# Kernel tuning notes

Measured on AMD Instinct MI355X. Metric: run time of the kernel, lower is better.

Reference implementation:

```python
import jax, jax.numpy as jnp
import numpy as np

A_BITS = 4          # a_bits
W_BITS = 4          # w_bits / w_slices (w_slices = 1)
NUM_CHUNKS = 9      # ceil(in_ch*9 / 64) = ceil(576/64)
BN_EPS = 1e-5


def quantize_weight(w, bits):
    # WeightQuantize STE: uniform symmetric quantization, straight-through on clipped range
    n = 2.0 ** (bits - 1) - 1.0
    c = jnp.clip(w, -1.0, 1.0)
    q = jnp.round(c * n) / n
    return c + jax.lax.stop_gradient(q - c)


def create_input_stream(a, a_bits):
    # residual multi-bit binarization into a_bits sign planes, x ~= sum_i plane_i / 2^(i+1)
    x = jnp.clip(a, -1.0, 1.0)
    planes = []
    r = x
    for i in range(a_bits):
        s = jnp.where(r >= 0, 1.0, -1.0)
        planes.append(x + jax.lax.stop_gradient(s - x))  # STE plane
        r = r - s / (2.0 ** (i + 1))
    return jnp.stack(planes, 0)  # [a_bits, B, C*9, L]


def unfold3x3(x, pad=1):
    # torch F.unfold(kernel=3, stride=1) ordering: (C, kh, kw) flattened channel-major
    B, C, H, W = x.shape
    xp = jnp.pad(x, ((0, 0), (0, 0), (pad, pad), (pad, pad)))
    cols = jnp.stack([xp[:, :, i:i + H, j:j + W] for i in range(3) for j in range(3)], axis=2)
    return cols.reshape(B, C * 9, H * W)  # [B, C*9, L]


def mtj(x, gamma, beta, key):
    mean = x.mean(axis=(0, 2), keepdims=True)
    var = x.var(axis=(0, 2), keepdims=True)  # biased, as torch BN
    normed = (x - mean) / jnp.sqrt(var + BN_EPS) * gamma[None, :, None] + beta[None, :, None]
    t = jnp.tanh(4.0 * normed)
    rand = jax.random.uniform(key, x.shape, minval=-1.0, maxval=1.0)
    out = jnp.where(t > rand, 1.0, -1.0)
    out = jnp.where(normed == 0.0, 0.0, out)
    c = jnp.clip(normed, -1.0, 1.0)
    return c + jax.lax.stop_gradient(out - c)


def setup_inputs() -> dict:
    key = jax.random.key(0)
    k1, k2 = jax.random.split(key)
    inputs = jax.random.normal(k1, (8, 64, 32, 32), dtype=jnp.float32)
    weight = jax.random.normal(k2, (128, 64, 3, 3), dtype=jnp.float32) * (2.0 / (64 * 9)) ** 0.5
    gamma = jnp.ones((128,), jnp.float32)
    beta = jnp.zeros((128,), jnp.float32)
    return {"inputs": inputs, "weight": weight, "gamma": gamma, "beta": beta}


def reference(inputs, weight, gamma, beta):
    O = weight.shape[0]
    # weight standardization (per output filter; std is unbiased as torch .std())
    wf = weight.reshape(O, -1)
    bw = weight - wf.mean(-1)[:, None, None, None]
    std = bw.reshape(O, -1).std(-1, ddof=1)
    bw = bw / std[:, None, None, None]
    qw = quantize_weight(bw, W_BITS)                      # [O, C, 3, 3]
    a = unfold3x3(inputs)                                 # [B, C*9, L]
    stream = create_input_stream(a, A_BITS)               # [A, B, C*9, L]
    A, B, CK, L = stream.shape
    cs = CK // NUM_CHUNKS
    x = stream.reshape(A * B, NUM_CHUNKS, cs, L)          # chunked along the C*9 axis
    fw = qw.reshape(O, NUM_CHUNKS, cs)                    # flattened weight chunks
    # per-chunk F.linear, vectorized over chunks: [nc, A*B, O, L]
    lt = jnp.einsum('ngkl,ogk->gnol', x, fw)
    keys = jax.random.split(jax.random.key(42), NUM_CHUNKS)
    pre = jax.vmap(lambda t, k: mtj(t, gamma, beta, k))(lt, keys) / NUM_CHUNKS
    out = pre.sum(0)                                      # sum chunks (w_slices=1 -> identity combine)
    # gen_image_vector_and_sum: recombine activation bit-planes
    out = out.reshape(A, B, O, L)
    wts = (2.0 ** -(jnp.arange(A, dtype=jnp.float32) + 1.0)).reshape(A, 1, 1, 1)
    out = (out * wts).sum(0)
    HW = int(np.sqrt(L))
    return out.reshape(B, O, HW, HW)                      # F.fold with (1,1) kernel
```

## Files before the change

### kernel.cpp

```cpp
#include <hip/hip_runtime.h>
#include <stdint.h>

#ifndef PRNG_PARTITIONABLE
#define PRNG_PARTITIONABLE 1
#endif

#define ONE_M_U 0.99999994039535522461f

__device__ __forceinline__ void tf_4a(uint32_t& x0, uint32_t& x1){
  x0 += x1; x1 = (x1<<13)|(x1>>19); x1 ^= x0;
  x0 += x1; x1 = (x1<<15)|(x1>>17); x1 ^= x0;
  x0 += x1; x1 = (x1<<26)|(x1>>6);  x1 ^= x0;
  x0 += x1; x1 = (x1<<6) |(x1>>26); x1 ^= x0;
}
__device__ __forceinline__ void tf_4b(uint32_t& x0, uint32_t& x1){
  x0 += x1; x1 = (x1<<17)|(x1>>15); x1 ^= x0;
  x0 += x1; x1 = (x1<<29)|(x1>>3);  x1 ^= x0;
  x0 += x1; x1 = (x1<<16)|(x1>>16); x1 ^= x0;
  x0 += x1; x1 = (x1<<24)|(x1>>8);  x1 ^= x0;
}
__device__ __forceinline__ void threefry2x32(uint32_t k0, uint32_t k1, uint32_t& x0, uint32_t& x1){
  uint32_t k2 = k0 ^ k1 ^ 0x1BD11BDAu;
  x0 += k0; x1 += k1;
  tf_4a(x0,x1); x0 += k1; x1 += k2 + 1u;
  tf_4b(x0,x1); x0 += k2; x1 += k0 + 2u;
  tf_4a(x0,x1); x0 += k0; x1 += k1 + 3u;
  tf_4b(x0,x1); x0 += k1; x1 += k2 + 4u;
  tf_4a(x0,x1); x0 += k2; x1 += k0 + 5u;
}

__device__ __forceinline__ float bits_to_unit(uint32_t b){
  #pragma clang fp contract(off)
  float f = __uint_as_float((b >> 9) | 0x3f800000u) - 1.0f;
  float r = f * 2.0f + (-1.0f);
  return __builtin_fmaxf(-1.0f, r);
}

__device__ __forceinline__ float xla_tanh_f32(float x){
  #pragma clang fp contract(off)
  float ax = __builtin_fabsf(x);
  float xc = __builtin_fminf(__builtin_fmaxf(x, -9.0f), 9.0f);
  float x2 = xc * xc;
  float nm = -2.76076847742355e-16f;
  nm = x2 * nm + 2.00018790482477e-13f;
  nm = x2 * nm + -8.60467152213735e-11f;
  nm = x2 * nm + 5.12229709037114e-08f;
  nm = x2 * nm + 1.48572235717979e-05f;
  nm = x2 * nm + 6.37261928875436e-04f;
  nm = x2 * nm + 4.89352455891786e-03f;
  nm = xc * nm;
  float dn = 1.19825839466702e-06f;
  dn = x2 * dn + 1.18534705686654e-04f;
  dn = x2 * dn + 2.26843463243900e-03f;
  dn = x2 * dn + 4.89352518554385e-03f;
  float res = nm / dn;
  return (ax < 0.0004f) ? x : res;
}

__device__ __forceinline__ float dot64(unsigned long long sw, unsigned long long dw,
                                       const float* w){
  float acc = 0.0f;
  #pragma unroll
  for (int k = 0; k < 64; ++k){
    float mag = ((dw >> k) & 1ull) ? ONE_M_U : 1.0f;
    float p   = ((sw >> k) & 1ull) ? mag : -mag;
    acc = __builtin_fmaf(p, w[k], acc);
  }
  return acc;
}

#define QW_OFF   0u
#define SGN_OFF  294912u
#define DIM_OFF  2654208u
#define KEYS_OFF 5013504u
#define MV_OFF   5013632u
#define LT_OFF   5023744u
#define LT_BYTES 150994944u
#define PART_OFF (LT_OFF + LT_BYTES)
#define PART_BYTES 2359296u
#define WS_NEEDED_FAST (PART_OFF + PART_BYTES)

__global__ __launch_bounds__(256) void k_front(const float* __restrict__ X,
        const float* __restrict__ W, float* __restrict__ qw, uint32_t* __restrict__ keys,
        unsigned long long* __restrict__ sgn, unsigned long long* __restrict__ dimw){
  #pragma clang fp contract(off)
  __shared__ float  bwL[576];
  __shared__ double red[64];
  int bx = blockIdx.x;
  int t = threadIdx.x;
  if (bx < 288){
    int g = bx >> 5;
    int tid = (bx & 31) * 256 + t;
    int b = tid >> 10, l = tid & 1023;
    int h = l >> 5, w = l & 31;
    unsigned long long sw0=0ull, sw1=0ull, sw2=0ull, sw3=0ull;
    unsigned long long dw0=0ull, dw1=0ull, dw2=0ull, dw3=0ull;
    const float* Xb = X + b*64*1024;
    int ck0 = g*64;
    #pragma unroll
    for (int i = 0; i < 64; ++i){
      int ck = ck0 + i;
      int c = ck / 9, kp = ck % 9;
      int di = kp / 3 - 1, dj = kp % 3 - 1;
      int hh = h + di, ww = w + dj;
      float v = 0.0f;
      if (hh >= 0 && hh < 32 && ww >= 0 && ww < 32)
        v = Xb[(c*32 + hh)*32 + ww];
      float x = __builtin_fminf(__builtin_fmaxf(v, -1.0f), 1.0f);
      float r = x;
      {
        float sv = (r >= 0.0f) ? 1.0f : -1.0f;
        float d  = sv - x; float p = x + d;
        if (sv > 0.0f) sw0 |= (1ull << i);
        if (__builtin_fabsf(p) < 1.0f) dw0 |= (1ull << i);
        r = r - sv * 0.5f;
      }
      {
        float sv = (r >= 0.0f) ? 1.0f : -1.0f;
        float d  = sv - x; float p = x + d;
        if (sv > 0.0f) sw1 |= (1ull << i);
        if (__builtin_fabsf(p) < 1.0f) dw1 |= (1ull << i);
        r = r - sv * 0.25f;
      }
      {
        float sv = (r >= 0.0f) ? 1.0f : -1.0f;
        float d  = sv - x; float p = x + d;
        if (sv > 0.0f) sw2 |= (1ull << i);
        if (__builtin_fabsf(p) < 1.0f) dw2 |= (1ull << i);
        r = r - sv * 0.125f;
      }
      {
        float sv = (r >= 0.0f) ? 1.0f : -1.0f;
        float d  = sv - x; float p = x + d;
        if (sv > 0.0f) sw3 |= (1ull << i);
        if (__builtin_fabsf(p) < 1.0f) dw3 |= (1ull << i);
        r = r - sv * 0.0625f;
      }
    }
    sgn [((0*8+b)*9 + g)*1024 + l] = sw0;
    sgn [((1*8+b)*9 + g)*1024 + l] = sw1;
    sgn [((2*8+b)*9 + g)*1024 + l] = sw2;
    sgn [((3*8+b)*9 + g)*1024 + l] = sw3;
    dimw[((0*8+b)*9 + g)*1024 + l] = dw0;
    dimw[((1*8+b)*9 + g)*1024 + l] = dw1;
    dimw[((2*8+b)*9 + g)*1024 + l] = dw2;
    dimw[((3*8+b)*9 + g)*1024 + l] = dw3;
  } else {
    int o = bx - 288;
    if (t < 64){
      double s = 0.0;
      for (int j = t; j < 576; j += 64) s += (double)W[o*576 + j];
      red[t] = s;
    }
    __syncthreads();
    for (int k = 32; k > 0; k >>= 1){ if (t < k) red[t] += red[t+k]; __syncthreads(); }
    float mean1 = (float)(red[0] / 576.0);
    __syncthreads();
    for (int j = t; j < 576; j += 256) bwL[j] = W[o*576 + j] - mean1;
    __syncthreads();
    if (t < 64){
      double s = 0.0;
      for (int j = t; j < 576; j += 64) s += (double)bwL[j];
      red[t] = s;
    }
    __syncthreads();
    for (int k = 32; k > 0; k >>= 1){ if (t < k) red[t] += red[t+k]; __syncthreads(); }
    float mean2 = (float)(red[0] / 576.0);
    __syncthreads();
    if (t < 64){
      double s = 0.0;
      for (int j = t; j < 576; j += 64){ float c = bwL[j] - mean2; float sq = c * c; s += (double)sq; }
      red[t] = s;
    }
    __syncthreads();
    for (int k = 32; k > 0; k >>= 1){ if (t < k) red[t] += red[t+k]; __syncthreads(); }
    float varf = (float)(red[0] / 575.0);
    float stdv = __builtin_sqrtf(varf);
    __syncthreads();
    for (int j = t; j < 576; j += 256){
      float b2 = bwL[j] / stdv;
      float c  = __builtin_fminf(__builtin_fmaxf(b2, -1.0f), 1.0f);
      float q  = __builtin_rintf(c * 7.0f) / 7.0f;
      float fwd = c + (q - c);
      int g = j >> 6, k = j & 63;
      qw [(g*128 + o)*64 + k] = fwd;
    }
    if (o == 0 && t == 0){
#if PRNG_PARTITIONABLE
      for (int g = 0; g < 9; ++g){
        uint32_t x0 = 0u, x1 = (uint32_t)g;
        threefry2x32(0u, 42u, x0, x1);
        keys[2*g] = x0; keys[2*g+1] = x1;
      }
#else
      uint32_t outv[18];
      for (int i = 0; i < 9; ++i){
        uint32_t x0 = (uint32_t)i, x1 = (uint32_t)(9 + i);
        threefry2x32(0u, 42u, x0, x1);
        outv[i] = x0; outv[9+i] = x1;
      }
      for (int j = 0; j < 18; ++j) keys[j] = outv[j];
#endif
    }
  }
}

__global__ __launch_bounds__(256) void k_gemm(const float* __restrict__ qw,
        const unsigned long long* __restrict__ sgn, const unsigned long long* __restrict__ dimw,
        float* __restrict__ lt, double* __restrict__ part){
  __shared__ float4 wS[128*17];
  __shared__ float4 pS[128*17];
  int lq = blockIdx.x, g = blockIdx.y, n = blockIdx.z;
  int t = threadIdx.x;
  {
    int o = t >> 4, kq = t & 15;
    const float4* qw4 = (const float4*)qw;
    #pragma unroll
    for (int i = 0; i < 8; ++i){
      int oo = o + 16*i;
      wS[oo*17 + kq] = qw4[(g*128 + oo)*16 + kq];
    }
  }
  {
    int l = t >> 1, kh = t & 1;
    unsigned long long sw = sgn [(n*9+g)*1024 + lq*128 + l];
    unsigned long long dw = dimw[(n*9+g)*1024 + lq*128 + l];
    #pragma unroll
    for (int kq = 0; kq < 8; ++kq){
      int kqq = kh*8 + kq;
      float4 v;
      {
        int k = kqq*4;
        float m0 = ((dw>>k)&1ull)?ONE_M_U:1.0f; v.x = ((sw>>k)&1ull)?m0:-m0;
        float m1 = ((dw>>(k+1))&1ull)?ONE_M_U:1.0f; v.y = ((sw>>(k+1))&1ull)?m1:-m1;
        float m2 = ((dw>>(k+2))&1ull)?ONE_M_U:1.0f; v.z = ((sw>>(k+2))&1ull)?m2:-m2;
        float m3 = ((dw>>(k+3))&1ull)?ONE_M_U:1.0f; v.w = ((sw>>(k+3))&1ull)?m3:-m3;
      }
      pS[l*17 + kqq] = v;
    }
  }
  __syncthreads();
  int ot = t >> 4, ltl = t & 15;
  float acc[8][8];
  #pragma unroll
  for (int i = 0; i < 8; ++i)
    #pragma unroll
    for (int j = 0; j < 8; ++j) acc[i][j] = 0.0f;
  for (int kq = 0; kq < 16; ++kq){
    float wr[8][4], pr[8][4];
    #pragma unroll
    for (int i = 0; i < 8; ++i) *(float4*)wr[i] = wS[(ot*8+i)*17 + kq];
    #pragma unroll
    for (int j = 0; j < 8; ++j) *(float4*)pr[j] = pS[(ltl+16*j)*17 + kq];
    #pragma unroll
    for (int e = 0; e < 4; ++e)
      #pragma unroll
      for (int i = 0; i < 8; ++i)
        #pragma unroll
        for (int j = 0; j < 8; ++j)
          acc[i][j] = __builtin_fmaf(pr[j][e], wr[i][e], acc[i][j]);
  }
  #pragma unroll
  for (int i = 0; i < 8; ++i){
    int o = ot*8 + i;
    float* dst = lt + ((size_t)((n*9+g)*128 + o))*1024 + lq*128 + ltl;
    #pragma unroll
    for (int j = 0; j < 8; ++j) dst[16*j] = acc[i][j];
  }
  double ps[8];
  #pragma unroll
  for (int i = 0; i < 8; ++i){
    double s = 0.0;
    #pragma unroll
    for (int j = 0; j < 8; ++j) s += (double)acc[i][j];
    ps[i] = s;
  }
  __syncthreads();
  double* red = (double*)pS;
  #pragma unroll
  for (int i = 0; i < 8; ++i) red[(ot*8+i)*16 + ltl] = ps[i];
  __syncthreads();
  if (t < 128){
    double s = 0.0;
    #pragma unroll
    for (int q = 0; q < 16; ++q) s += red[t*16 + q];
    part[((size_t)g*128 + t)*256 + n*8 + lq] = s;
  }
}

__global__ __launch_bounds__(256) void k_stats(const float* __restrict__ lt,
        const double* __restrict__ part, float* __restrict__ mv){
  #pragma clang fp contract(off)
  __shared__ double redm[64];
  __shared__ double red[256];
  __shared__ float meanS;
  int go = blockIdx.x;
  int g = go >> 7, o = go & 127;
  int t = threadIdx.x;
  if (t < 64){
    double s = 0.0;
    for (int idx = t; idx < 256; idx += 64) s += part[(size_t)go*256 + idx];
    redm[t] = s;
  }
  __syncthreads();
  for (int k = 32; k > 0; k >>= 1){ if (t < k) redm[t] += redm[t+k]; __syncthreads(); }
  if (t == 0){
    float mean = (float)(redm[0] / 32768.0);
    mv[go*2] = mean;
    meanS = mean;
  }
  __syncthreads();
  float mean = meanS;
  double s2 = 0.0;
  #pragma unroll 8
  for (int n = 0; n < 32; ++n){
    const float4* p4 = (const float4*)(lt + ((size_t)((n*9+g)*128 + o)) * 1024);
    float4 v = p4[t];
    { float c = v.x - mean; float sq = c * c; s2 += (double)sq; }
    { float c = v.y - mean; float sq = c * c; s2 += (double)sq; }
    { float c = v.z - mean; float sq = c * c; s2 += (double)sq; }
    { float c = v.w - mean; float sq = c * c; s2 += (double)sq; }
  }
  red[t] = s2; __syncthreads();
  for (int k = 128; k > 0; k >>= 1){ if (t < k) red[t] += red[t+k]; __syncthreads(); }
  if (t == 0){
    float var = (float)(red[0] / 32768.0);
    mv[go*2 + 1] = __builtin_sqrtf(var + 1e-5f);
  }
}

__global__ __launch_bounds__(256) void k_out_fast(const float* __restrict__ lt,
        const float* __restrict__ mv, const uint32_t* __restrict__ keys,
        const float* __restrict__ gamma, const float* __restrict__ beta,
        float* __restrict__ out){
  #pragma clang fp contract(off)
  __shared__ float    mvL[18];
  __shared__ uint32_t kL[18];
  int bi = blockIdx.x;
  int lc = bi & 3, o = (bi >> 2) & 127, b = bi >> 9;
  int t = threadIdx.x;
  if (t < 18){ mvL[t] = mv[((t>>1)*128 + o)*2 + (t&1)]; kL[t] = keys[t]; }
  __syncthreads();
  int l = lc*256 + t;
  float gma = gamma[o], bta = beta[o];
  float S[4] = {0.0f, 0.0f, 0.0f, 0.0f};
  for (int g = 0; g < 9; ++g){
    float rnd[4];
#if PRNG_PARTITIONABLE
    #pragma unroll
    for (int a = 0; a < 4; ++a){
      uint32_t m = (uint32_t)((a*8 + b)*131072 + o*1024 + l);
      uint32_t x0 = 0u, x1 = m;
      threefry2x32(kL[2*g], kL[2*g+1], x0, x1);
      rnd[a] = bits_to_unit(x0 ^ x1);
    }
#else
    #pragma unroll
    for (int a01 = 0; a01 < 2; ++a01){
      uint32_t m = (uint32_t)((a01*8 + b)*131072 + o*1024 + l);
      uint32_t x0 = m, x1 = m + 2097152u;
      threefry2x32(kL[2*g], kL[2*g+1], x0, x1);
      rnd[a01]     = bits_to_unit(x0);
      rnd[a01 + 2] = bits_to_unit(x1);
    }
#endif
    float mean = mvL[2*g], den = mvL[2*g+1];
    #pragma unroll
    for (int a = 0; a < 4; ++a){
      int n = a*8 + b;
      float tv = lt[((size_t)((n*9+g)*128 + o)) * 1024 + l];
      float normed = (tv - mean) / den * gma + bta;
      float th = xla_tanh_f32(4.0f * normed);
      float dec = (th > rnd[a]) ? 1.0f : -1.0f;
      if (normed == 0.0f) dec = 0.0f;
      float cc  = __builtin_fminf(__builtin_fmaxf(normed, -1.0f), 1.0f);
      float fwd = cc + (dec - cc);
      float pre = fwd / 9.0f;
      S[a] = S[a] + pre;
    }
  }
  float z = S[0] * 0.5f;
  z = z + S[1] * 0.25f;
  z = z + S[2] * 0.125f;
  z = z + S[3] * 0.0625f;
  out[(b*128 + o)*1024 + l] = z;
}

__global__ __launch_bounds__(256) void k_stats_slow(const float* __restrict__ qw,
        const unsigned long long* __restrict__ sgn, const unsigned long long* __restrict__ dimw,
        float* __restrict__ mv){
  #pragma clang fp contract(off)
  __shared__ double red[256];
  int g = blockIdx.x >> 7, o = blockIdx.x & 127, t = threadIdx.x;
  float wr[64];
  #pragma unroll
  for (int k = 0; k < 64; ++k) wr[k] = qw[(g*128 + o)*64 + k];
  double s1 = 0.0;
  for (int n = 0; n < 32; ++n){
    const unsigned long long* sp = sgn  + (n*9 + g)*1024;
    const unsigned long long* dp = dimw + (n*9 + g)*1024;
    for (int j = 0; j < 4; ++j){
      int l = t + j*256;
      float tvv = dot64(sp[l], dp[l], wr);
      s1 += (double)tvv;
    }
  }
  red[t] = s1; __syncthreads();
  for (int k = 128; k > 0; k >>= 1){ if (t < k) red[t] += red[t+k]; __syncthreads(); }
  float mean = (float)(red[0] / 32768.0);
  __syncthreads();
  double s2 = 0.0;
  for (int n = 0; n < 32; ++n){
    const unsigned long long* sp = sgn  + (n*9 + g)*1024;
    const unsigned long long* dp = dimw + (n*9 + g)*1024;
    for (int j = 0; j < 4; ++j){
      int l = t + j*256;
      float tvv = dot64(sp[l], dp[l], wr);
      float c = tvv - mean;
      float sq = c * c;
      s2 += (double)sq;
    }
  }
  red[t] = s2; __syncthreads();
  for (int k = 128; k > 0; k >>= 1){ if (t < k) red[t] += red[t+k]; __syncthreads(); }
  if (t == 0){
    float var = (float)(red[0] / 32768.0);
    float den = __builtin_sqrtf(var + 1e-5f);
    mv[(g*128+o)*2]   = mean;
    mv[(g*128+o)*2+1] = den;
  }
}

__global__ __launch_bounds__(256) void k_out_slow(const float* __restrict__ qw,
        const unsigned long long* __restrict__ sgn, const unsigned long long* __restrict__ dimw,
        const float* __restrict__ mv, const uint32_t* __restrict__ keys,
        const float* __restrict__ gamma, const float* __restrict__ beta,
        float* __restrict__ out){
  #pragma clang fp contract(off)
  __shared__ float    wv[576];
  __shared__ float    mvL[18];
  __shared__ uint32_t kL[18];
  int bi = blockIdx.x;
  int lc = bi & 3, o = (bi >> 2) & 127, b = bi >> 9;
  int t = threadIdx.x;
  for (int j = t; j < 576; j += 256) wv[j] = qw[((j >> 6)*128 + o)*64 + (j & 63)];
  if (t < 18){ mvL[t] = mv[((t>>1)*128 + o)*2 + (t&1)]; kL[t] = keys[t]; }
  __syncthreads();
  int l = lc*256 + t;
  float gma = gamma[o], bta = beta[o];
  float S[4] = {0.0f, 0.0f, 0.0f, 0.0f};
  for (int g = 0; g < 9; ++g){
    float rnd[4];
#if PRNG_PARTITIONABLE
    #pragma unroll
    for (int a = 0; a < 4; ++a){
      uint32_t m = (uint32_t)((a*8 + b)*131072 + o*1024 + l);
      uint32_t x0 = 0u, x1 = m;
      threefry2x32(kL[2*g], kL[2*g+1], x0, x1);
      rnd[a] = bits_to_unit(x0 ^ x1);
    }
#else
    #pragma unroll
    for (int a01 = 0; a01 < 2; ++a01){
      uint32_t m = (uint32_t)((a01*8 + b)*131072 + o*1024 + l);
      uint32_t x0 = m, x1 = m + 2097152u;
      threefry2x32(kL[2*g], kL[2*g+1], x0, x1);
      rnd[a01]     = bits_to_unit(x0);
      rnd[a01 + 2] = bits_to_unit(x1);
    }
#endif
    float mean = mvL[2*g], den = mvL[2*g+1];
    float wr[64];
    #pragma unroll
    for (int k = 0; k < 64; ++k) wr[k] = wv[g*64 + k];
    #pragma unroll
    for (int a = 0; a < 4; ++a){
      int n = a*8 + b;
      float tvv = dot64(sgn[(n*9+g)*1024 + l], dimw[(n*9+g)*1024 + l], wr);
      float normed = (tvv - mean) / den * gma + bta;
      float th = xla_tanh_f32(4.0f * normed);
      float dec = (th > rnd[a]) ? 1.0f : -1.0f;
      if (normed == 0.0f) dec = 0.0f;
      float cc  = __builtin_fminf(__builtin_fmaxf(normed, -1.0f), 1.0f);
      float fwd = cc + (dec - cc);
      float pre = fwd / 9.0f;
      S[a] = S[a] + pre;
    }
  }
  float z = S[0] * 0.5f;
  z = z + S[1] * 0.25f;
  z = z + S[2] * 0.125f;
  z = z + S[3] * 0.0625f;
  out[(b*128 + o)*1024 + l] = z;
}

extern "C" void kernel_launch(void* const* d_in, const int* in_sizes, int n_in,
                              void* d_out, int out_size, void* d_ws, size_t ws_size,
                              hipStream_t stream){
  (void)in_sizes; (void)n_in; (void)out_size;
  const float* inp   = (const float*)d_in[0];
  const float* wgt   = (const float*)d_in[1];
  const float* gamma = (const float*)d_in[2];
  const float* beta  = (const float*)d_in[3];
  float* out = (float*)d_out;
  char* ws = (char*)d_ws;
  float*              qw    = (float*)(ws + QW_OFF);
  unsigned long long* sgn   = (unsigned long long*)(ws + SGN_OFF);
  unsigned long long* dimw  = (unsigned long long*)(ws + DIM_OFF);
  uint32_t*           keys  = (uint32_t*)(ws + KEYS_OFF);
  float*              mv    = (float*)(ws + MV_OFF);
  float*              lt    = (float*)(ws + LT_OFF);
  double*             part  = (double*)(ws + PART_OFF);

  hipLaunchKernelGGL(k_front, dim3(416), dim3(256), 0, stream, inp, wgt, qw, keys, sgn, dimw);
  if (ws_size >= (size_t)WS_NEEDED_FAST){
    hipLaunchKernelGGL(k_gemm,     dim3(8, 9, 32), dim3(256), 0, stream, qw, sgn, dimw, lt, part);
    hipLaunchKernelGGL(k_stats,    dim3(1152),     dim3(256), 0, stream, lt, part, mv);
    hipLaunchKernelGGL(k_out_fast, dim3(4096),     dim3(256), 0, stream, lt, mv, keys,
                       gamma, beta, out);
  } else {
    hipLaunchKernelGGL(k_stats_slow, dim3(1152), dim3(256), 0, stream, qw, sgn, dimw, mv);
    hipLaunchKernelGGL(k_out_slow,   dim3(4096), dim3(256), 0, stream, qw, sgn, dimw, mv, keys,
                       gamma, beta, out);
  }
}
```

Baseline: 290.7 us.

## Fuse sum-of-squares into GEMM epilogue and drop the lt re-read stats pass

The GEMM epilogue now accumulates per-channel sums of squares in double precision alongside the sums, and a tiny k_den kernel computes variance as E[x^2]-mean^2. This removes the k_stats pass that re-read the whole 151MB lt buffer to compute centered variance. The GEMM also halves the pS shared tile by decoding the bit-planes in two K halves, and adds a min-blocks occupancy hint. The one-pass variance formula can lose precision compared with the two-pass centered form, which may matter for exact agreement with the reference.

New measurement: 273.9 us. -5.8%, faster.

```diff
diff --git a/kernel.cpp b/kernel.cpp
--- a/kernel.cpp
+++ b/kernel.cpp
@@ -76,9 +76,10 @@
 #define MV_OFF   5013632u
 #define LT_OFF   5023744u
 #define LT_BYTES 150994944u
-#define PART_OFF (LT_OFF + LT_BYTES)
+#define PART_OFF  (LT_OFF + LT_BYTES)
 #define PART_BYTES 2359296u
-#define WS_NEEDED_FAST (PART_OFF + PART_BYTES)
+#define PART2_OFF (PART_OFF + PART_BYTES)
+#define WS_NEEDED_FAST (PART2_OFF + PART_BYTES)
 
 __global__ __launch_bounds__(256) void k_front(const float* __restrict__ X,
         const float* __restrict__ W, float* __restrict__ qw, uint32_t* __restrict__ keys,
@@ -205,11 +206,11 @@
   }
 }
 
-__global__ __launch_bounds__(256) void k_gemm(const float* __restrict__ qw,
+__global__ __launch_bounds__(256, 3) void k_gemm(const float* __restrict__ qw,
         const unsigned long long* __restrict__ sgn, const unsigned long long* __restrict__ dimw,
-        float* __restrict__ lt, double* __restrict__ part){
+        float* __restrict__ lt, double* __restrict__ part, double* __restrict__ part2){
   __shared__ float4 wS[128*17];
-  __shared__ float4 pS[128*17];
+  __shared__ float4 pS[128*9];
   int lq = blockIdx.x, g = blockIdx.y, n = blockIdx.z;
   int t = threadIdx.x;
   {
@@ -221,44 +222,45 @@
       wS[oo*17 + kq] = qw4[(g*128 + oo)*16 + kq];
     }
   }
-  {
-    int l = t >> 1, kh = t & 1;
-    unsigned long long sw = sgn [(n*9+g)*1024 + lq*128 + l];
-    unsigned long long dw = dimw[(n*9+g)*1024 + lq*128 + l];
-    #pragma unroll
-    for (int kq = 0; kq < 8; ++kq){
-      int kqq = kh*8 + kq;
-      float4 v;
-      {
-        int k = kqq*4;
-        float m0 = ((dw>>k)&1ull)?ONE_M_U:1.0f; v.x = ((sw>>k)&1ull)?m0:-m0;
-        float m1 = ((dw>>(k+1))&1ull)?ONE_M_U:1.0f; v.y = ((sw>>(k+1))&1ull)?m1:-m1;
-        float m2 = ((dw>>(k+2))&1ull)?ONE_M_U:1.0f; v.z = ((sw>>(k+2))&1ull)?m2:-m2;
-        float m3 = ((dw>>(k+3))&1ull)?ONE_M_U:1.0f; v.w = ((sw>>(k+3))&1ull)?m3:-m3;
-      }
-      pS[l*17 + kqq] = v;
-    }
-  }
-  __syncthreads();
+  int lde = t >> 1, kh = t & 1;
+  unsigned long long sw = sgn [(n*9+g)*1024 + lq*128 + lde];
+  unsigned long long dw = dimw[(n*9+g)*1024 + lq*128 + lde];
   int ot = t >> 4, ltl = t & 15;
   float acc[8][8];
   #pragma unroll
   for (int i = 0; i < 8; ++i)
     #pragma unroll
     for (int j = 0; j < 8; ++j) acc[i][j] = 0.0f;
-  for (int kq = 0; kq < 16; ++kq){
-    float wr[8][4], pr[8][4];
-    #pragma unroll
-    for (int i = 0; i < 8; ++i) *(float4*)wr[i] = wS[(ot*8+i)*17 + kq];
-    #pragma unroll
-    for (int j = 0; j < 8; ++j) *(float4*)pr[j] = pS[(ltl+16*j)*17 + kq];
-    #pragma unroll
-    for (int e = 0; e < 4; ++e)
+  #pragma unroll
+  for (int h = 0; h < 2; ++h){
+    #pragma unroll
+    for (int q = 0; q < 4; ++q){
+      int kq2 = kh*4 + q;
+      int k = (h*8 + kq2)*4;
+      float4 v;
+      float m0 = ((dw>>k)&1ull)?ONE_M_U:1.0f;     v.x = ((sw>>k)&1ull)?m0:-m0;
+      float m1 = ((dw>>(k+1))&1ull)?ONE_M_U:1.0f; v.y = ((sw>>(k+1))&1ull)?m1:-m1;
+      float m2 = ((dw>>(k+2))&1ull)?ONE_M_U:1.0f; v.z = ((sw>>(k+2))&1ull)?m2:-m2;
+      float m3 = ((dw>>(k+3))&1ull)?ONE_M_U:1.0f; v.w = ((sw>>(k+3))&1ull)?m3:-m3;
+      pS[lde*9 + kq2] = v;
+    }
+    __syncthreads();
+    for (int kq2 = 0; kq2 < 8; ++kq2){
+      int kq = h*8 + kq2;
+      float wr[8][4], pr[8][4];
       #pragma unroll
-      for (int i = 0; i < 8; ++i)
+      for (int i = 0; i < 8; ++i) *(float4*)wr[i] = wS[(ot*8+i)*17 + kq];
+      #pragma unroll
+      for (int j = 0; j < 8; ++j) *(float4*)pr[j] = pS[(ltl+16*j)*9 + kq2];
+      #pragma unroll
+      for (int e = 0; e < 4; ++e)
         #pragma unroll
-        for (int j = 0; j < 8; ++j)
-          acc[i][j] = __builtin_fmaf(pr[j][e], wr[i][e], acc[i][j]);
+        for (int i = 0; i < 8; ++i)
+          #pragma unroll
+          for (int j = 0; j < 8; ++j)
+            acc[i][j] = __builtin_fmaf(pr[j][e], wr[i][e], acc[i][j]);
+    }
+    __syncthreads();
   }
   #pragma unroll
   for (int i = 0; i < 8; ++i){
@@ -267,18 +269,21 @@
     #pragma unroll
     for (int j = 0; j < 8; ++j) dst[16*j] = acc[i][j];
   }
-  double ps[8];
+  double ps1[8], ps2[8];
   #pragma unroll
   for (int i = 0; i < 8; ++i){
-    double s = 0.0;
-    #pragma unroll
-    for (int j = 0; j < 8; ++j) s += (double)acc[i][j];
-    ps[i] = s;
-  }
-  __syncthreads();
+    double s1 = 0.0, s2 = 0.0;
+    #pragma unroll
+    for (int j = 0; j < 8; ++j){
+      double d = (double)acc[i][j];
+      s1 += d;
+      s2 += d * d;
+    }
+    ps1[i] = s1; ps2[i] = s2;
+  }
   double* red = (double*)pS;
   #pragma unroll
-  for (int i = 0; i < 8; ++i) red[(ot*8+i)*16 + ltl] = ps[i];
+  for (int i = 0; i < 8; ++i) red[(ot*8+i)*16 + ltl] = ps1[i];
   __syncthreads();
   if (t < 128){
     double s = 0.0;
@@ -286,46 +291,41 @@
     for (int q = 0; q < 16; ++q) s += red[t*16 + q];
     part[((size_t)g*128 + t)*256 + n*8 + lq] = s;
   }
-}
-
-__global__ __launch_bounds__(256) void k_stats(const float* __restrict__ lt,
-        const double* __restrict__ part, float* __restrict__ mv){
-  #pragma clang fp contract(off)
+  __syncthreads();
+  #pragma unroll
+  for (int i = 0; i < 8; ++i) red[(ot*8+i)*16 + ltl] = ps2[i];
+  __syncthreads();
+  if (t < 128){
+    double s = 0.0;
+    #pragma unroll
+    for (int q = 0; q < 16; ++q) s += red[t*16 + q];
+    part2[((size_t)g*128 + t)*256 + n*8 + lq] = s;
+  }
+}
+
+__global__ __launch_bounds__(64) void k_den(const double* __restrict__ part,
+        const double* __restrict__ part2, float* __restrict__ mv){
   __shared__ double redm[64];
-  __shared__ double red[256];
-  __shared__ float meanS;
-  int go = blockIdx.x;
-  int g = go >> 7, o = go & 127;
-  int t = threadIdx.x;
-  if (t < 64){
-    double s = 0.0;
-    for (int idx = t; idx < 256; idx += 64) s += part[(size_t)go*256 + idx];
-    redm[t] = s;
-  }
-  __syncthreads();
-  for (int k = 32; k > 0; k >>= 1){ if (t < k) redm[t] += redm[t+k]; __syncthreads(); }
+  __shared__ double redv[64];
+  int go = blockIdx.x, t = threadIdx.x;
+  double s = 0.0;
+  for (int idx = t; idx < 256; idx += 64) s += part[(size_t)go*256 + idx];
+  redm[t] = s;
+  double v = 0.0;
+  for (int idx = t; idx < 256; idx += 64) v += part2[(size_t)go*256 + idx];
+  redv[t] = v;
+  __syncthreads();
+  for (int k = 32; k > 0; k >>= 1){
+    if (t < k){ redm[t] += redm[t+k]; redv[t] += redv[t+k]; }
+    __syncthreads();
+  }
   if (t == 0){
     float mean = (float)(redm[0] / 32768.0);
     mv[go*2] = mean;
-    meanS = mean;
-  }
-  __syncthreads();
-  float mean = meanS;
-  double s2 = 0.0;
-  #pragma unroll 8
-  for (int n = 0; n < 32; ++n){
-    const float4* p4 = (const float4*)(lt + ((size_t)((n*9+g)*128 + o)) * 1024);
-    float4 v = p4[t];
-    { float c = v.x - mean; float sq = c * c; s2 += (double)sq; }
-    { float c = v.y - mean; float sq = c * c; s2 += (double)sq; }
-    { float c = v.z - mean; float sq = c * c; s2 += (double)sq; }
-    { float c = v.w - mean; float sq = c * c; s2 += (double)sq; }
-  }
-  red[t] = s2; __syncthreads();
-  for (int k = 128; k > 0; k >>= 1){ if (t < k) red[t] += red[t+k]; __syncthreads(); }
-  if (t == 0){
-    float var = (float)(red[0] / 32768.0);
-    mv[go*2 + 1] = __builtin_sqrtf(var + 1e-5f);
+    double m = (double)mean;
+    double var64 = (redv[0] - 2.0*m*redm[0] + 32768.0*m*m) / 32768.0;
+    float varf = (float)var64;
+    mv[go*2 + 1] = __builtin_sqrtf(varf + 1e-5f);
   }
 }
 
@@ -511,11 +511,13 @@
   float*              mv    = (float*)(ws + MV_OFF);
   float*              lt    = (float*)(ws + LT_OFF);
   double*             part  = (double*)(ws + PART_OFF);
+  double*             part2 = (double*)(ws + PART2_OFF);
 
   hipLaunchKernelGGL(k_front, dim3(416), dim3(256), 0, stream, inp, wgt, qw, keys, sgn, dimw);
   if (ws_size >= (size_t)WS_NEEDED_FAST){
-    hipLaunchKernelGGL(k_gemm,     dim3(8, 9, 32), dim3(256), 0, stream, qw, sgn, dimw, lt, part);
-    hipLaunchKernelGGL(k_stats,    dim3(1152),     dim3(256), 0, stream, lt, part, mv);
+    hipLaunchKernelGGL(k_gemm,     dim3(8, 9, 32), dim3(256), 0, stream, qw, sgn, dimw,
+                       lt, part, part2);
+    hipLaunchKernelGGL(k_den,      dim3(1152),     dim3(64),  0, stream, part, part2, mv);
     hipLaunchKernelGGL(k_out_fast, dim3(4096),     dim3(256), 0, stream, lt, mv, keys,
                        gamma, beta, out);
   } else {
```
